# Optimization experiments

Measured on AMD Instinct MI355X. Metric: run time of the kernel, lower is better.

## Reference

```python
import jax, jax.numpy as jnp
import numpy as np

N, C, T, V, H = 64, 256, 64, 25, 8


def setup_inputs() -> dict:
    key = jax.random.key(0)
    ks = jax.random.split(key, 6)
    s = 1.0 / np.sqrt(C)
    x = jax.random.normal(ks[0], (N, C, T, V), dtype=jnp.float32)
    Wqkv = jax.random.normal(ks[1], (3 * C, C), dtype=jnp.float32) * s
    bqkv = jax.random.normal(ks[2], (3 * C,), dtype=jnp.float32) * 0.01
    Wproj = jax.random.normal(ks[3], (C, C), dtype=jnp.float32) * s
    bproj = jax.random.normal(ks[4], (C,), dtype=jnp.float32) * 0.01
    hop_w = jnp.array([0.1], dtype=jnp.float32)
    idx = jnp.arange(V, dtype=jnp.float32)
    hop_grid = jnp.abs(idx[:, None] - idx[None, :])  # [V,V] hop distances
    return {"x": x, "Wqkv": Wqkv, "bqkv": bqkv, "Wproj": Wproj,
            "bproj": bproj, "hop_w": hop_w, "hop_grid": hop_grid}


def reference(x, Wqkv, bqkv, Wproj, bproj, hop_w, hop_grid):
    n, c, t, v = x.shape
    d = c // H
    scale = d ** -0.5
    # 1x1 conv == per-(t,v) linear over channels
    qkv = jnp.einsum('nctv,oc->notv', x, Wqkv) + bqkv[None, :, None, None]
    qkv = qkv.reshape(n, 3, H, d, t, v)
    q, k, val = qkv[:, 0], qkv[:, 1], qkv[:, 2]  # [n,H,d,t,v]
    # scores over joints per frame: [n,t,H,v,v]
    attn = jnp.einsum('nhdtv,nhdtu->nthvu', q, k) * scale
    attn = attn - hop_w[0] * hop_grid  # additive hop-distance bias
    attn = jax.nn.softmax(attn, axis=-1)
    x_att = jnp.einsum('nthvu,nhdtu->nhdtv', attn, val).reshape(n, c, t, v)
    out = jnp.einsum('nctv,oc->notv', x_att, Wproj) + bproj[None, :, None, None]
    return out + x
```

## Files before the change

### kernel.cpp

```cpp
#include <hip/hip_runtime.h>


typedef short bf16x8 __attribute__((ext_vector_type(8)));
typedef short short4v __attribute__((ext_vector_type(4)));
typedef float f32x4 __attribute__((ext_vector_type(4)));

__device__ __forceinline__ unsigned short f2bf(float f) {
  union { float f; unsigned u; } v; v.f = f;
  unsigned r = v.u + 0x7fffu + ((v.u >> 16) & 1u);
  return (unsigned short)(r >> 16);
}
__device__ __forceinline__ float bf2f(unsigned short s) {
  union { unsigned u; float f; } v; v.u = ((unsigned)s) << 16;
  return v.f;
}

__global__ void convert_weights(const float* __restrict__ wqkv,
                                const float* __restrict__ wproj,
                                unsigned short* __restrict__ wout) {
  int i = blockIdx.x * blockDim.x + threadIdx.x;
  const int total = 768 * 256 + 256 * 256;
  for (; i < total; i += gridDim.x * blockDim.x) {
    float f = (i < 768 * 256) ? wqkv[i] : wproj[i - 768 * 256];
    wout[i] = f2bf(f);
  }
}

#define SWZ(tok, e) ((e) ^ (((tok) & 7) << 3))

__global__ __launch_bounds__(512, 4)
void phys_attn_fused(const float* __restrict__ x,
                     const float* __restrict__ bqkv,
                     const float* __restrict__ bproj,
                     const float* __restrict__ hop_w,
                     const float* __restrict__ hop_grid,
                     const unsigned short* __restrict__ wbf,
                     float* __restrict__ out) {
  __shared__ unsigned short x_tok[32 * 256];
  __shared__ unsigned short xatt[32 * 256];
  __shared__ unsigned short qk_t[32 * 264];
  __shared__ unsigned short val_s[128 * 40];
  __shared__ unsigned short p_s[8 * 16 * 40];
  __shared__ float pen[32 * 33];

  const int tid = threadIdx.x;
  const int b = blockIdx.x;
  const int n = b >> 6, t = b & 63;
  const int w = tid >> 6;
  const int lane = tid & 63;
  const int l15 = lane & 15, lg = lane >> 4;

  const unsigned short* Wq = wbf;
  const unsigned short* Wp = wbf + 768 * 256;

  {
    const float* xb = x + (size_t)n * 409600 + (size_t)t * 25;
    for (int idx = tid; idx < 1792; idx += 512) {
      int r = 25 + (idx >> 8), c = idx & 255;
      x_tok[SWZ(r, r * 256 + c)] = 0;
    }
#pragma unroll 4
    for (int i = tid; i < 6400; i += 512) {
      int c = i / 25;
      int v = i - c * 25;
      x_tok[SWZ(v, v * 256 + c)] = f2bf(xb[c * 1600 + v]);
    }
    float hw = hop_w[0];
    for (int i = tid; i < 1024; i += 512) {
      int v = i >> 5, u = i & 31;
      float pv = (u < 25) ? ((v < 25) ? hw * hop_grid[v * 25 + u] : 0.0f)
                          : __builtin_inff();
      pen[v * 33 + u] = pv;
    }
  }
  __syncthreads();

  const float scale = 0.17677669529663687f;

  for (int g = 0; g < 2; ++g) {
#pragma unroll
    for (int j = 0; j < 6; ++j) {
      int tIdx = w * 6 + j;
      int mt = tIdx >> 1, nt = tIdx & 1;
      int sec = mt >> 3;
      int rem = mt & 7;
      int hh = rem >> 1;
      int sub = rem & 1;
      int wrow0 = sec * 256 + (g * 4 + hh) * 32 + sub * 16;
      int tok = nt * 16 + l15;
      f32x4 acc = {0.f, 0.f, 0.f, 0.f};
      int arow = (wrow0 + l15) * 256 + lg * 8;
      int brow = tok * 256 + lg * 8;
#pragma unroll
      for (int ks = 0; ks < 8; ++ks) {
        bf16x8 a = *(const bf16x8*)(Wq + arow + ks * 32);
        bf16x8 bfr = *(const bf16x8*)(x_tok + SWZ(tok, brow + ks * 32));
        acc = __builtin_amdgcn_mfma_f32_16x16x32_bf16(a, bfr, acc, 0, 0, 0);
      }
      int rb = wrow0 + lg * 4;
      unsigned short h0 = f2bf(acc[0] + bqkv[rb + 0]);
      unsigned short h1 = f2bf(acc[1] + bqkv[rb + 1]);
      unsigned short h2 = f2bf(acc[2] + bqkv[rb + 2]);
      unsigned short h3 = f2bf(acc[3] + bqkv[rb + 3]);
      if (sec < 2) {
        int op = sec * 128 + hh * 32 + sub * 16 + lg * 4;
        short4v pk = {(short)h0, (short)h1, (short)h2, (short)h3};
        *(short4v*)(qk_t + tok * 264 + op) = pk;
      } else {
        int dd = hh * 32 + sub * 16 + lg * 4;
        val_s[(dd + 0) * 40 + tok] = h0;
        val_s[(dd + 1) * 40 + tok] = h1;
        val_s[(dd + 2) * 40 + tok] = h2;
        val_s[(dd + 3) * 40 + tok] = h3;
      }
    }
    __syncthreads();

    {
      int hh = w >> 1;
      int vbase = (w & 1) * 16;
      int hglob = g * 4 + hh;
      bf16x8 aq = *(const bf16x8*)(qk_t + (vbase + l15) * 264 + hh * 32 + lg * 8);
      f32x4 att0, att1;
      {
        f32x4 z = {0.f, 0.f, 0.f, 0.f};
        bf16x8 bk0 = *(const bf16x8*)(qk_t + (0 + l15) * 264 + 128 + hh * 32 + lg * 8);
        att0 = __builtin_amdgcn_mfma_f32_16x16x32_bf16(aq, bk0, z, 0, 0, 0);
        bf16x8 bk1 = *(const bf16x8*)(qk_t + (16 + l15) * 264 + 128 + hh * 32 + lg * 8);
        att1 = __builtin_amdgcn_mfma_f32_16x16x32_bf16(aq, bk1, z, 0, 0, 0);
      }
      int pbase = w * 640;
#pragma unroll
      for (int r = 0; r < 4; ++r) {
        int v = vbase + lg * 4 + r;
        float f0 = att0[r] * scale - pen[v * 33 + l15];
        float f1 = att1[r] * scale - pen[v * 33 + 16 + l15];
        float m = fmaxf(f0, f1);
        m = fmaxf(m, __shfl_xor(m, 1));
        m = fmaxf(m, __shfl_xor(m, 2));
        m = fmaxf(m, __shfl_xor(m, 4));
        m = fmaxf(m, __shfl_xor(m, 8));
        float e0 = __expf(f0 - m);
        float e1 = __expf(f1 - m);
        float s = e0 + e1;
        s += __shfl_xor(s, 1);
        s += __shfl_xor(s, 2);
        s += __shfl_xor(s, 4);
        s += __shfl_xor(s, 8);
        float inv = 1.0f / s;
        p_s[pbase + (lg * 4 + r) * 40 + l15] = f2bf(e0 * inv);
        p_s[pbase + (lg * 4 + r) * 40 + 16 + l15] = f2bf(e1 * inv);
      }
      bf16x8 bp = *(const bf16x8*)(p_s + pbase + l15 * 40 + lg * 8);
#pragma unroll
      for (int mt2 = 0; mt2 < 2; ++mt2) {
        bf16x8 av = *(const bf16x8*)(val_s + (hh * 32 + mt2 * 16 + l15) * 40 + lg * 8);
        f32x4 z = {0.f, 0.f, 0.f, 0.f};
        f32x4 o = __builtin_amdgcn_mfma_f32_16x16x32_bf16(av, bp, z, 0, 0, 0);
        int c0 = hglob * 32 + mt2 * 16 + lg * 4;
        int tok = vbase + l15;
        short4v pk = {(short)f2bf(o[0]), (short)f2bf(o[1]),
                      (short)f2bf(o[2]), (short)f2bf(o[3])};
        *(short4v*)(xatt + SWZ(tok, tok * 256 + c0)) = pk;
      }
    }
    __syncthreads();
  }

#pragma unroll
  for (int j = 0; j < 4; ++j) {
    int tIdx = w * 4 + j;
    int mt = tIdx >> 1, nt = tIdx & 1;
    int tok = nt * 16 + l15;
    f32x4 acc = {0.f, 0.f, 0.f, 0.f};
    int arow = (mt * 16 + l15) * 256 + lg * 8;
    int brow = tok * 256 + lg * 8;
#pragma unroll
    for (int ks = 0; ks < 8; ++ks) {
      bf16x8 a = *(const bf16x8*)(Wp + arow + ks * 32);
      bf16x8 bfr = *(const bf16x8*)(xatt + SWZ(tok, brow + ks * 32));
      acc = __builtin_amdgcn_mfma_f32_16x16x32_bf16(a, bfr, acc, 0, 0, 0);
    }
    if (tok < 25) {
      int o0 = mt * 16 + lg * 4;
      short4v xr = *(const short4v*)(x_tok + SWZ(tok, tok * 256 + o0));
      float* op = out + (size_t)n * 409600 + (size_t)t * 25 + tok;
      op[(size_t)(o0 + 0) * 1600] = acc[0] + bproj[o0 + 0] + bf2f((unsigned short)xr[0]);
      op[(size_t)(o0 + 1) * 1600] = acc[1] + bproj[o0 + 1] + bf2f((unsigned short)xr[1]);
      op[(size_t)(o0 + 2) * 1600] = acc[2] + bproj[o0 + 2] + bf2f((unsigned short)xr[2]);
      op[(size_t)(o0 + 3) * 1600] = acc[3] + bproj[o0 + 3] + bf2f((unsigned short)xr[3]);
    }
  }
}

extern "C" void kernel_launch(void* const* d_in, const int* in_sizes, int n_in,
                              void* d_out, int out_size, void* d_ws, size_t ws_size,
                              hipStream_t stream) {
  const float* x        = (const float*)d_in[0];
  const float* wqkv     = (const float*)d_in[1];
  const float* bqkv     = (const float*)d_in[2];
  const float* wproj    = (const float*)d_in[3];
  const float* bproj    = (const float*)d_in[4];
  const float* hop_w    = (const float*)d_in[5];
  const float* hop_grid = (const float*)d_in[6];
  float* out = (float*)d_out;
  unsigned short* wbf = (unsigned short*)d_ws;

  convert_weights<<<dim3(256), dim3(256), 0, stream>>>(wqkv, wproj, wbf);
  phys_attn_fused<<<dim3(64 * 64), dim3(512), 0, stream>>>(
      x, bqkv, bproj, hop_w, hop_grid, wbf, out);
}
```

Baseline: 617.9 us.

## Split input transpose and output epilogue into separate coalesced kernels

Adds a pre-pass kernel that transposes x from channel-major fp32 into a token-major bf16 buffer with the swizzle applied, and a finish kernel that transposes the projection result back and adds bias and the fp32 residual with coalesced float4 accesses. The fused kernel now loads its token tile directly into LDS with global_load_lds and writes bf16 output rows into the same buffer in place. The goal is to replace the strided 1600-element gathers and scatters in the main kernel with coalesced traffic. The cost is two extra launches and an extra bf16 round trip through global memory. The residual now uses full-precision x, and in-place reuse of xt is safe because each block reads and writes only its own tokens.

```diff
diff --git a/kernel.cpp b/kernel.cpp
--- a/kernel.cpp
+++ b/kernel.cpp
@@ -4,6 +4,8 @@
 typedef short bf16x8 __attribute__((ext_vector_type(8)));
 typedef short short4v __attribute__((ext_vector_type(4)));
 typedef float f32x4 __attribute__((ext_vector_type(4)));
+
+#define XT_ELEMS (64ull * 1600ull * 256ull)
 
 __device__ __forceinline__ unsigned short f2bf(float f) {
   union { float f; unsigned u; } v; v.f = f;
@@ -13,6 +15,12 @@
 __device__ __forceinline__ float bf2f(unsigned short s) {
   union { unsigned u; float f; } v; v.u = ((unsigned)s) << 16;
   return v.f;
+}
+
+__device__ __forceinline__ void gload_lds16(const void* g, void* l) {
+  __builtin_amdgcn_global_load_lds(
+      (const __attribute__((address_space(1))) unsigned int*)g,
+      (__attribute__((address_space(3))) unsigned int*)l, 16, 0, 0);
 }
 
 __global__ void convert_weights(const float* __restrict__ wqkv,
@@ -28,14 +36,78 @@
 
 #define SWZ(tok, e) ((e) ^ (((tok) & 7) << 3))
 
+__global__ __launch_bounds__(512)
+void k0_transpose(const float* __restrict__ x, unsigned short* __restrict__ xt) {
+  __shared__ unsigned short T[160 * 136];
+  int b = blockIdx.x;
+  int tc = b % 10, ch = (b / 10) & 1, n = b / 20;
+  int tok0 = tc * 160, c0 = ch * 128;
+  int tid = threadIdx.x;
+  int c = c0 + (tid >> 2), tq = tid & 3;
+  const float* xrow = x + ((size_t)(n * 256 + c)) * 1600 + tok0 + tq * 40;
+#pragma unroll
+  for (int i = 0; i < 40; i += 4) {
+    float4 f = *(const float4*)(xrow + i);
+    int tl = tq * 40 + i;
+    int tokg = tok0 + tl;
+    float vals[4] = {f.x, f.y, f.z, f.w};
+#pragma unroll
+    for (int j = 0; j < 4; ++j) {
+      int v = (tokg + j) % 25;
+      int csw = c ^ ((v & 7) << 3);
+      T[(tl + j) * 136 + (csw - c0)] = f2bf(vals[j]);
+    }
+  }
+  __syncthreads();
+#pragma unroll
+  for (int k = 0; k < 5; ++k) {
+    int u = tid + k * 512;
+    int tl = u >> 4, j = u & 15;
+    bf16x8 w = *(const bf16x8*)(&T[tl * 136 + j * 8]);
+    *(bf16x8*)(xt + ((size_t)n * 1600 + tok0 + tl) * 256 + c0 + j * 8) = w;
+  }
+}
+
+__global__ __launch_bounds__(512)
+void k4_finish(const unsigned short* __restrict__ ot, const float* __restrict__ x,
+               const float* __restrict__ bproj, float* __restrict__ out) {
+  __shared__ unsigned short T[160 * 136];
+  int b = blockIdx.x;
+  int tc = b % 10, ch = (b / 10) & 1, n = b / 20;
+  int tok0 = tc * 160, c0 = ch * 128;
+  int tid = threadIdx.x;
+#pragma unroll
+  for (int k = 0; k < 5; ++k) {
+    int u = tid + k * 512;
+    int tl = u >> 4, j = u & 15;
+    bf16x8 w = *(const bf16x8*)(ot + ((size_t)n * 1600 + tok0 + tl) * 256 + c0 + j * 8);
+    *(bf16x8*)(&T[tl * 136 + j * 8]) = w;
+  }
+  __syncthreads();
+  int c = c0 + (tid >> 2), tq = tid & 3;
+  float bp = bproj[c];
+  const float* xr = x + ((size_t)(n * 256 + c)) * 1600 + tok0 + tq * 40;
+  float* orow = out + ((size_t)(n * 256 + c)) * 1600 + tok0 + tq * 40;
+  int cc = c - c0;
+#pragma unroll
+  for (int i = 0; i < 40; i += 4) {
+    float4 xv = *(const float4*)(xr + i);
+    int tl = tq * 40 + i;
+    float4 r;
+    r.x = bf2f(T[(tl + 0) * 136 + cc]) + bp + xv.x;
+    r.y = bf2f(T[(tl + 1) * 136 + cc]) + bp + xv.y;
+    r.z = bf2f(T[(tl + 2) * 136 + cc]) + bp + xv.z;
+    r.w = bf2f(T[(tl + 3) * 136 + cc]) + bp + xv.w;
+    *(float4*)(orow + i) = r;
+  }
+}
+
 __global__ __launch_bounds__(512, 4)
-void phys_attn_fused(const float* __restrict__ x,
-                     const float* __restrict__ bqkv,
-                     const float* __restrict__ bproj,
+void phys_attn_fused(const float* __restrict__ bqkv,
                      const float* __restrict__ hop_w,
                      const float* __restrict__ hop_grid,
                      const unsigned short* __restrict__ wbf,
-                     float* __restrict__ out) {
+                     unsigned short* __restrict__ xt) {
   __shared__ unsigned short x_tok[32 * 256];
   __shared__ unsigned short xatt[32 * 256];
   __shared__ unsigned short qk_t[32 * 264];
@@ -54,16 +126,9 @@
   const unsigned short* Wp = wbf + 768 * 256;
 
   {
-    const float* xb = x + (size_t)n * 409600 + (size_t)t * 25;
-    for (int idx = tid; idx < 1792; idx += 512) {
-      int r = 25 + (idx >> 8), c = idx & 255;
-      x_tok[SWZ(r, r * 256 + c)] = 0;
-    }
-#pragma unroll 4
-    for (int i = tid; i < 6400; i += 512) {
-      int c = i / 25;
-      int v = i - c * 25;
-      x_tok[SWZ(v, v * 256 + c)] = f2bf(xb[c * 1600 + v]);
+    for (int idx = tid; idx < 7 * 256; idx += 512) {
+      int r = 25 + (idx >> 8);
+      x_tok[r * 256 + (idx & 255)] = 0;
     }
     float hw = hop_w[0];
     for (int i = tid; i < 1024; i += 512) {
@@ -72,6 +137,13 @@
                           : __builtin_inff();
       pen[v * 33 + u] = pv;
     }
+    const char* src = (const char*)(xt + ((size_t)n * 1600 + t * 25) * 256);
+    char* dst = (char*)x_tok;
+    int base = w * 1024;
+    gload_lds16(src + base + lane * 16, dst + base);
+    int base2 = base + 8192;
+    if (base2 + lane * 16 < 12800)
+      gload_lds16(src + base2 + lane * 16, dst + base2);
   }
   __syncthreads();
 
@@ -177,18 +249,15 @@
     int brow = tok * 256 + lg * 8;
 #pragma unroll
     for (int ks = 0; ks < 8; ++ks) {
-      bf16x8 a = *(const bf16x8*)(Wp + arow + ks * 32);
+      bf16x8 a = *(const bf16x8*)(Wp + arow + ks * 8 * 4);
       bf16x8 bfr = *(const bf16x8*)(xatt + SWZ(tok, brow + ks * 32));
       acc = __builtin_amdgcn_mfma_f32_16x16x32_bf16(a, bfr, acc, 0, 0, 0);
     }
     if (tok < 25) {
       int o0 = mt * 16 + lg * 4;
-      short4v xr = *(const short4v*)(x_tok + SWZ(tok, tok * 256 + o0));
-      float* op = out + (size_t)n * 409600 + (size_t)t * 25 + tok;
-      op[(size_t)(o0 + 0) * 1600] = acc[0] + bproj[o0 + 0] + bf2f((unsigned short)xr[0]);
-      op[(size_t)(o0 + 1) * 1600] = acc[1] + bproj[o0 + 1] + bf2f((unsigned short)xr[1]);
-      op[(size_t)(o0 + 2) * 1600] = acc[2] + bproj[o0 + 2] + bf2f((unsigned short)xr[2]);
-      op[(size_t)(o0 + 3) * 1600] = acc[3] + bproj[o0 + 3] + bf2f((unsigned short)xr[3]);
+      short4v pk = {(short)f2bf(acc[0]), (short)f2bf(acc[1]),
+                    (short)f2bf(acc[2]), (short)f2bf(acc[3])};
+      *(short4v*)(xt + ((size_t)n * 1600 + t * 25 + tok) * 256 + o0) = pk;
     }
   }
 }
@@ -204,9 +273,13 @@
   const float* hop_w    = (const float*)d_in[5];
   const float* hop_grid = (const float*)d_in[6];
   float* out = (float*)d_out;
-  unsigned short* wbf = (unsigned short*)d_ws;
+
+  unsigned short* xt  = (unsigned short*)d_ws;
+  unsigned short* wbf = (unsigned short*)d_ws + XT_ELEMS;
 
   convert_weights<<<dim3(256), dim3(256), 0, stream>>>(wqkv, wproj, wbf);
+  k0_transpose<<<dim3(1280), dim3(512), 0, stream>>>(x, xt);
   phys_attn_fused<<<dim3(64 * 64), dim3(512), 0, stream>>>(
-      x, bqkv, bproj, hop_w, hop_grid, wbf, out);
-}
+      bqkv, hop_w, hop_grid, wbf, xt);
+  k4_finish<<<dim3(1280), dim3(512), 0, stream>>>(xt, x, bproj, out);
+}
```

After: 651.1 us. 1.05x slower.
